# Kernel tuning notes

Measured on AMD Instinct MI355X. Metric: run time of the kernel, lower is better.

Reference implementation:

```python
import jax, jax.numpy as jnp
import numpy as np
import math

SEQ_LEN = 720
PRED_LEN = 720
CHANNELS = 862
BATCH = 64
IN_LEN = SEQ_LEN // 2  # seq_len is even -> no padding branch


def dct2_ortho_matrix(N):
    # Orthonormal DCT-II matrix D so that dct(x, norm='ortho') = x @ D.T along last axis
    n = jnp.arange(N, dtype=jnp.float32)
    k = n[:, None]
    D = jnp.cos(jnp.pi * (n[None, :] + 0.5) * k / N) * jnp.sqrt(2.0 / N)
    D = D.at[0].multiply(1.0 / jnp.sqrt(2.0))
    return D  # [N, N], row k = frequency k


def setup_inputs() -> dict:
    key = jax.random.key(0)
    ks = jax.random.split(key, 7)
    x = jax.random.normal(ks[0], (BATCH, SEQ_LEN, CHANNELS), dtype=jnp.float32)
    # depthwise 1x1 convs == per-channel scale + bias
    w1 = jax.random.normal(ks[1], (CHANNELS,), dtype=jnp.float32) * 0.1
    b1 = jax.random.normal(ks[2], (CHANNELS,), dtype=jnp.float32) * 0.1
    w2 = jax.random.normal(ks[3], (CHANNELS,), dtype=jnp.float32) * 0.1
    b2 = jax.random.normal(ks[4], (CHANNELS,), dtype=jnp.float32) * 0.1
    # Linear(in_len, pred_len): W [pred_len, in_len], b [pred_len]
    W_lo = jax.random.normal(ks[5], (PRED_LEN, IN_LEN), dtype=jnp.float32) / math.sqrt(IN_LEN)
    b_lo = jax.random.normal(ks[6], (PRED_LEN,), dtype=jnp.float32) * 0.01
    return {"x": x, "w1": w1, "b1": b1, "w2": w2, "b2": b2, "W_lo": W_lo, "b_lo": b_lo}


def reference(x, w1, b1, w2, b2, W_lo, b_lo):
    B, L, C = x.shape
    xt = jnp.transpose(x, (0, 2, 1))              # [B, C, L]
    seq_mean = jnp.mean(xt, axis=-1, keepdims=True)
    xt = xt - seq_mean
    # depthwise low-pass conv, kernel [1,1]/sqrt(2), stride 2
    lp = xt.reshape(B, C, L // 2, 2).sum(-1) / jnp.sqrt(jnp.float32(2.0))  # [B, C, N]
    N = L // 2
    D = dct2_ortho_matrix(N)
    xd = jnp.einsum('bcn,kn->bck', lp, D) / N     # DCT-II ortho along last axis, scaled
    # x += conv1x1_1(conv1x1_2(x)) -- depthwise 1x1 convs are per-channel affine
    y = (xd * w2[:, None] + b2[:, None]) * w1[:, None] + b1[:, None]
    xd = xd + y
    out = jnp.einsum('bcn,pn->bcp', xd, W_lo) + b_lo  # Linear(in_len -> pred_len)
    out = out + seq_mean                           # [B, C, pred_len]
    return jnp.transpose(out, (0, 2, 1))           # [B, pred_len, C]
```

## Files before the change

kernel.cpp:

```cpp
#include <hip/hip_runtime.h>
#include <hip/hip_bf16.h>
#include <cstdint>

#define SEQ   720
#define PRED  720
#define CH    862
#define NB    64
#define NIN   360
#define KP    384
#define CP    896
#define PP    768
#define BK    32

typedef __attribute__((ext_vector_type(8))) short s16x8;
typedef __attribute__((ext_vector_type(4))) float f32x4;
typedef __attribute__((ext_vector_type(2))) float f32x2;
typedef unsigned int u32;
typedef unsigned short u16;

__device__ __forceinline__ u16 to_bf16u(float f){
  __hip_bfloat16 h = __float2bfloat16(f);
  return *reinterpret_cast<u16*>(&h);
}

__global__ __launch_bounds__(256) void k_dct(float* __restrict__ Dm){
  int idx = blockIdx.x*256 + threadIdx.x;
  if (idx >= NIN*NIN) return;
  int n = idx / NIN, m = idx % NIN;
  int r = ((2*m+1)*n) % (4*NIN);
  float ang = (float)r * (float)(3.14159265358979323846 / 720.0);
  float v = cosf(ang) * 0.07453559924999299f;
  if (n == 0) v *= 0.7071067811865476f;
  Dm[idx] = v;
}

__global__ __launch_bounds__(384) void k_mmat(const float* __restrict__ Wlo, const float* __restrict__ Dm,
                                              u16* __restrict__ Mbf, float* __restrict__ Srow,
                                              float* __restrict__ Slo){
  int p = blockIdx.x;
  int t = threadIdx.x;
  if (p >= PRED){
    Mbf[(size_t)p*KP + t] = 0;
    if (t == 0){ Srow[p] = 0.f; Slo[p] = 0.f; }
    return;
  }
  __shared__ float Wrow[NIN];
  __shared__ float redM[6], redW[6];
  if (t < NIN) Wrow[t] = Wlo[(size_t)p*NIN + t];
  __syncthreads();
  float acc = 0.f;
  if (t < NIN){
    const float* Dc = Dm + t;
    #pragma unroll 4
    for (int n = 0; n < NIN; n++) acc += Wrow[n] * Dc[(size_t)n*NIN];
    acc *= (1.0f/360.0f);
  }
  Mbf[(size_t)p*KP + t] = (t < NIN) ? to_bf16u(acc) : (u16)0;
  float mv = (t < NIN) ? acc : 0.f;
  float wv = (t < NIN) ? Wrow[t] : 0.f;
  #pragma unroll
  for (int off = 32; off > 0; off >>= 1){
    mv += __shfl_down(mv, off);
    wv += __shfl_down(wv, off);
  }
  int wid = t >> 6, lid = t & 63;
  if (lid == 0){ redM[wid] = mv; redW[wid] = wv; }
  __syncthreads();
  if (t == 0){
    float sm = 0.f, sw = 0.f;
    #pragma unroll
    for (int i = 0; i < 6; i++){ sm += redM[i]; sw += redW[i]; }
    Srow[p] = sm; Slo[p] = sw;
  }
}

__global__ __launch_bounds__(256) void k_pre(const float* __restrict__ x, u16* __restrict__ pairB,
                                             float* __restrict__ meanw){
  int b  = blockIdx.y;
  int c0 = blockIdx.x * 64;
  int t  = threadIdx.x;
  int c16  = t & 15;
  int mrow = t >> 4;
  int w    = t >> 6;
  __shared__ u16  pl[NIN][66];
  __shared__ float red[4][64];
  const float rs2 = 0.7071067811865476f;
  int cb = c0 + c16*4;
  bool full = (cb + 3 < CH);
  const float* xb = x + (size_t)b*SEQ*CH + cb;
  float s0=0.f, s1=0.f, s2=0.f, s3=0.f;

  for (int m = mrow; m < NIN; m += 16){
    const float* r0 = xb + (size_t)(2*m)*CH;
    float a0,a1,a2,a3, e0,e1,e2,e3;
    if (full){
      f32x4 va = *reinterpret_cast<const f32x4*>(r0);
      f32x2 vb = *reinterpret_cast<const f32x2*>(r0 + CH);
      f32x2 vc = *reinterpret_cast<const f32x2*>(r0 + CH + 2);
      a0=va.x; a1=va.y; a2=va.z; a3=va.w;
      e0=vb.x; e1=vb.y; e2=vc.x; e3=vc.y;
    } else {
      a0 = (cb+0<CH)? r0[0]:0.f; a1 = (cb+1<CH)? r0[1]:0.f;
      a2 = (cb+2<CH)? r0[2]:0.f; a3 = (cb+3<CH)? r0[3]:0.f;
      e0 = (cb+0<CH)? r0[CH+0]:0.f; e1 = (cb+1<CH)? r0[CH+1]:0.f;
      e2 = (cb+2<CH)? r0[CH+2]:0.f; e3 = (cb+3<CH)? r0[CH+3]:0.f;
    }
    float p0=a0+e0, p1=a1+e1, p2=a2+e2, p3=a3+e3;
    s0+=p0; s1+=p1; s2+=p2; s3+=p3;
    u32 lo = (u32)to_bf16u(p0*rs2) | ((u32)to_bf16u(p1*rs2) << 16);
    u32 hi = (u32)to_bf16u(p2*rs2) | ((u32)to_bf16u(p3*rs2) << 16);
    *reinterpret_cast<u32*>(&pl[m][c16*4 + 0]) = lo;
    *reinterpret_cast<u32*>(&pl[m][c16*4 + 2]) = hi;
  }

  s0 += __shfl_down(s0, 32); s1 += __shfl_down(s1, 32);
  s2 += __shfl_down(s2, 32); s3 += __shfl_down(s3, 32);
  s0 += __shfl_down(s0, 16); s1 += __shfl_down(s1, 16);
  s2 += __shfl_down(s2, 16); s3 += __shfl_down(s3, 16);
  if ((t & 63) < 16){
    f32x4 rv; rv.x=s0; rv.y=s1; rv.z=s2; rv.w=s3;
    *reinterpret_cast<f32x4*>(&red[w][c16*4]) = rv;
  }
  __syncthreads();
  if (t < 64){
    float mean = (red[0][t] + red[1][t] + red[2][t] + red[3][t]) * (1.0f/SEQ);
    meanw[(size_t)b*CP + c0 + t] = mean;
  }

  int rowc = t >> 2;
  int mq0  = t & 3;
  size_t rbase = ((size_t)b*CP + c0 + rowc) * KP;
  for (int i = 0; i < 12; i++){
    int mg = mq0 + 4*i;
    u16 vals[8];
    #pragma unroll
    for (int j = 0; j < 8; j++){
      int m = mg*8 + j;
      vals[j] = (m < NIN) ? pl[m][rowc] : (u16)0;
    }
    uint4 pk;
    pk.x = (u32)vals[0] | ((u32)vals[1] << 16);
    pk.y = (u32)vals[2] | ((u32)vals[3] << 16);
    pk.z = (u32)vals[4] | ((u32)vals[5] << 16);
    pk.w = (u32)vals[6] | ((u32)vals[7] << 16);
    *reinterpret_cast<uint4*>(pairB + rbase + (size_t)mg*8) = pk;
  }
}

#define GLOAD_LDS16(gp, lp_) __builtin_amdgcn_global_load_lds( \
    (const __attribute__((address_space(1))) u32*)(gp), \
    (__attribute__((address_space(3))) u32*)(lp_), 16, 0, 0)

__global__ __launch_bounds__(256, 4) void k_gemm(const u16* __restrict__ Apack, const u16* __restrict__ Mbf,
                                              const float* __restrict__ Srow, const float* __restrict__ Slo,
                                              const float* __restrict__ meanw,
                                              const float* __restrict__ w1, const float* __restrict__ b1,
                                              const float* __restrict__ w2, const float* __restrict__ b2,
                                              const float* __restrict__ blo,
                                              float* __restrict__ out){
  int bid = blockIdx.x;
  int idx = (bid & 7) * 336 + (bid >> 3);
  int pt  = idx % 6;
  int rem = idx / 6;
  int ct  = rem % 7;
  int b   = rem / 7;

  int t  = threadIdx.x;
  int w  = t >> 6, l = t & 63;
  int wr = w >> 1, wc = w & 1;

  __shared__ __align__(16) char smem[32768];
  u16 (*As)[128*BK] = reinterpret_cast<u16(*)[128*BK]>(smem);
  u16 (*Bs)[128*BK] = reinterpret_cast<u16(*)[128*BK]>(smem + 16384);
  float (*wbuf)[16][68] = reinterpret_cast<float(*)[16][68]>(smem);

  f32x4 acc[4][4] = {};

  const u16* Abase = Apack + ((size_t)b*CP + (size_t)ct*128) * KP;
  const u16* Bbase = Mbf + (size_t)pt*128*KP;
  int srow = t >> 2;
  int squad = t & 3;
  int row16 = l & 15, kb = l >> 4;
  int sperm = (srow >> 1) & 3;
  int rperm = (row16 >> 1) & 3;

#define STAGE(bufi, k0) do { \
    GLOAD_LDS16(Abase + (size_t)(srow)*KP + (k0) + ((squad^sperm))*8,      &As[bufi][(srow)*BK + squad*8]); \
    GLOAD_LDS16(Abase + (size_t)(64 + srow)*KP + (k0) + ((squad^sperm))*8, &As[bufi][(64 + srow)*BK + squad*8]); \
    GLOAD_LDS16(Bbase + (size_t)(srow)*KP + (k0) + ((squad^sperm))*8,      &Bs[bufi][(srow)*BK + squad*8]); \
    GLOAD_LDS16(Bbase + (size_t)(64 + srow)*KP + (k0) + ((squad^sperm))*8, &Bs[bufi][(64 + srow)*BK + squad*8]); \
  } while(0)

  STAGE(0, 0);
  for (int ks = 0; ks < 12; ks++){
    int cur = ks & 1;
    if (ks < 11){
      STAGE(cur ^ 1, (ks + 1) * BK);
      asm volatile("s_waitcnt vmcnt(4)" ::: "memory");
    } else {
      asm volatile("s_waitcnt vmcnt(0)" ::: "memory");
    }
    __builtin_amdgcn_s_barrier();
    s16x8 af[4], bfr[4];
    #pragma unroll
    for (int mi = 0; mi < 4; mi++)
      af[mi] = *reinterpret_cast<const s16x8*>(&As[cur][(wr*64 + mi*16 + row16)*BK + (kb^rperm)*8]);
    #pragma unroll
    for (int ni = 0; ni < 4; ni++)
      bfr[ni] = *reinterpret_cast<const s16x8*>(&Bs[cur][(wc*64 + ni*16 + row16)*BK + (kb^rperm)*8]);
    __builtin_amdgcn_s_setprio(1);
    #pragma unroll
    for (int mi = 0; mi < 4; mi++)
      #pragma unroll
      for (int ni = 0; ni < 4; ni++)
        acc[mi][ni] = __builtin_amdgcn_mfma_f32_16x16x32_bf16(af[mi], bfr[ni], acc[mi][ni], 0, 0, 0);
    __builtin_amdgcn_s_setprio(0);
    __builtin_amdgcn_s_barrier();
  }
  __syncthreads();

  int cq = l & 15, pg = l >> 4;
  int cb4 = ct*128 + wr*64 + cq*4;
  float sc4[4], of4[4], cn4[4];
  float bc4[4];
  #pragma unroll
  for (int j = 0; j < 4; j++){
    int c = cb4 + j;
    bool v = (c < CH);
    float w1v = v ? w1[c] : 0.f, w2v = v ? w2[c] : 0.f;
    float b1v = v ? b1[c] : 0.f, b2v = v ? b2[c] : 0.f;
    float mv  = v ? meanw[(size_t)b*CP + c] : 0.f;
    sc4[j] = 1.f + w1v*w2v;
    of4[j] = w1v*b2v + b1v;
    cn4[j] = mv;
    bc4[j] = 1.4142135623730951f * sc4[j] * mv;
  }
  bool cfull = (cb4 + 3 < CH);
  size_t outb = (size_t)b*PRED*CH;

  #pragma unroll
  for (int ni = 0; ni < 4; ni++){
    #pragma unroll
    for (int mi = 0; mi < 4; mi++){
      #pragma unroll
      for (int r = 0; r < 4; r++){
        wbuf[w][row16][mi*16 + kb*4 + r] = acc[mi][ni][r];
      }
    }
    int pbase = pt*128 + wc*64 + ni*16;
    #pragma unroll
    for (int q = 0; q < 4; q++){
      int pi = q*4 + pg;
      int p = pbase + pi;
      if (p < PRED){
        f32x4 g = *reinterpret_cast<const f32x4*>(&wbuf[w][pi][cq*4]);
        float sp = Srow[p], sl = Slo[p], bl = blo[p];
        f32x4 ov;
        #pragma unroll
        for (int j = 0; j < 4; j++)
          ov[j] = sc4[j]*g[j] + (cn4[j] - bc4[j]*sp + of4[j]*sl + bl);
        if (cfull){
          *reinterpret_cast<f32x4*>(&out[outb + (size_t)p*CH + cb4]) = ov;
        } else {
          #pragma unroll
          for (int j = 0; j < 4; j++)
            if (cb4 + j < CH) out[outb + (size_t)p*CH + cb4 + j] = ov[j];
        }
      }
    }
  }
}

extern "C" void kernel_launch(void* const* d_in, const int* in_sizes, int n_in,
                              void* d_out, int out_size, void* d_ws, size_t ws_size,
                              hipStream_t stream)
{
  const float* x   = (const float*)d_in[0];
  const float* w1  = (const float*)d_in[1];
  const float* b1  = (const float*)d_in[2];
  const float* w2  = (const float*)d_in[3];
  const float* b2  = (const float*)d_in[4];
  const float* Wlo = (const float*)d_in[5];
  const float* blo = (const float*)d_in[6];
  float* out = (float*)d_out;

  char* ws = (char*)d_ws;
  float* Dm    = (float*)(ws);
  u16*   Mbf   = (u16*)(ws + 518400);
  float* Srow  = (float*)(ws + 518400 + 589824);
  float* Slo   = (float*)(ws + 518400 + 589824 + 3072);
  u16*   pairB = (u16*)(ws + 518400 + 589824 + 6144);
  float* meanw = (float*)(ws + 518400 + 589824 + 6144 + 44040192);

  k_dct<<<dim3((NIN*NIN + 255)/256), dim3(256), 0, stream>>>(Dm);
  k_mmat<<<dim3(PP), dim3(384), 0, stream>>>(Wlo, Dm, Mbf, Srow, Slo);
  k_pre<<<dim3(CP/64, NB), dim3(256), 0, stream>>>(x, pairB, meanw);
  k_gemm<<<dim3(6*7*NB), dim3(256), 0, stream>>>(pairB, Mbf, Srow, Slo, meanw,
                                                 w1, b1, w2, b2, blo, out);
}
```

Measured before the change: 162.8 us.

## Fuse preprocessing into GEMM, keeping full-K activation tile resident in LDS

Merges the pairwise-sum/mean/bf16-pack kernel with the GEMM. Each 512-thread block now loads a 64-channel slice of one batch from x, keeps the whole 384-long K panel in XOR-swizzled LDS, and loops over three 256-wide output tiles, streaming only the DCT-Linear matrix. This removes the packed intermediate buffer round-trip through global memory and one launch. The cost is 80KB of LDS per block, which limits occupancy, plus a serial prologue whose global loads of x are scalar and cannot overlap with the MFMA work.

```diff
diff --git a/kernel.cpp b/kernel.cpp
--- a/kernel.cpp
+++ b/kernel.cpp
@@ -8,13 +8,11 @@
 #define NB    64
 #define NIN   360
 #define KP    384
-#define CP    896
 #define PP    768
-#define BK    32
+#define BKK   32
 
 typedef __attribute__((ext_vector_type(8))) short s16x8;
 typedef __attribute__((ext_vector_type(4))) float f32x4;
-typedef __attribute__((ext_vector_type(2))) float f32x2;
 typedef unsigned int u32;
 typedef unsigned short u16;
 
@@ -74,200 +72,184 @@
   }
 }
 
-__global__ __launch_bounds__(256) void k_pre(const float* __restrict__ x, u16* __restrict__ pairB,
-                                             float* __restrict__ meanw){
-  int b  = blockIdx.y;
-  int c0 = blockIdx.x * 64;
-  int t  = threadIdx.x;
-  int c16  = t & 15;
-  int mrow = t >> 4;
-  int w    = t >> 6;
-  __shared__ u16  pl[NIN][66];
-  __shared__ float red[4][64];
-  const float rs2 = 0.7071067811865476f;
-  int cb = c0 + c16*4;
-  bool full = (cb + 3 < CH);
-  const float* xb = x + (size_t)b*SEQ*CH + cb;
-  float s0=0.f, s1=0.f, s2=0.f, s3=0.f;
-
-  for (int m = mrow; m < NIN; m += 16){
-    const float* r0 = xb + (size_t)(2*m)*CH;
-    float a0,a1,a2,a3, e0,e1,e2,e3;
-    if (full){
-      f32x4 va = *reinterpret_cast<const f32x4*>(r0);
-      f32x2 vb = *reinterpret_cast<const f32x2*>(r0 + CH);
-      f32x2 vc = *reinterpret_cast<const f32x2*>(r0 + CH + 2);
-      a0=va.x; a1=va.y; a2=va.z; a3=va.w;
-      e0=vb.x; e1=vb.y; e2=vc.x; e3=vc.y;
-    } else {
-      a0 = (cb+0<CH)? r0[0]:0.f; a1 = (cb+1<CH)? r0[1]:0.f;
-      a2 = (cb+2<CH)? r0[2]:0.f; a3 = (cb+3<CH)? r0[3]:0.f;
-      e0 = (cb+0<CH)? r0[CH+0]:0.f; e1 = (cb+1<CH)? r0[CH+1]:0.f;
-      e2 = (cb+2<CH)? r0[CH+2]:0.f; e3 = (cb+3<CH)? r0[CH+3]:0.f;
-    }
-    float p0=a0+e0, p1=a1+e1, p2=a2+e2, p3=a3+e3;
-    s0+=p0; s1+=p1; s2+=p2; s3+=p3;
-    u32 lo = (u32)to_bf16u(p0*rs2) | ((u32)to_bf16u(p1*rs2) << 16);
-    u32 hi = (u32)to_bf16u(p2*rs2) | ((u32)to_bf16u(p3*rs2) << 16);
-    *reinterpret_cast<u32*>(&pl[m][c16*4 + 0]) = lo;
-    *reinterpret_cast<u32*>(&pl[m][c16*4 + 2]) = hi;
-  }
-
-  s0 += __shfl_down(s0, 32); s1 += __shfl_down(s1, 32);
-  s2 += __shfl_down(s2, 32); s3 += __shfl_down(s3, 32);
-  s0 += __shfl_down(s0, 16); s1 += __shfl_down(s1, 16);
-  s2 += __shfl_down(s2, 16); s3 += __shfl_down(s3, 16);
-  if ((t & 63) < 16){
-    f32x4 rv; rv.x=s0; rv.y=s1; rv.z=s2; rv.w=s3;
-    *reinterpret_cast<f32x4*>(&red[w][c16*4]) = rv;
-  }
-  __syncthreads();
-  if (t < 64){
-    float mean = (red[0][t] + red[1][t] + red[2][t] + red[3][t]) * (1.0f/SEQ);
-    meanw[(size_t)b*CP + c0 + t] = mean;
-  }
-
-  int rowc = t >> 2;
-  int mq0  = t & 3;
-  size_t rbase = ((size_t)b*CP + c0 + rowc) * KP;
-  for (int i = 0; i < 12; i++){
-    int mg = mq0 + 4*i;
-    u16 vals[8];
-    #pragma unroll
-    for (int j = 0; j < 8; j++){
-      int m = mg*8 + j;
-      vals[j] = (m < NIN) ? pl[m][rowc] : (u16)0;
-    }
-    uint4 pk;
-    pk.x = (u32)vals[0] | ((u32)vals[1] << 16);
-    pk.y = (u32)vals[2] | ((u32)vals[3] << 16);
-    pk.z = (u32)vals[4] | ((u32)vals[5] << 16);
-    pk.w = (u32)vals[6] | ((u32)vals[7] << 16);
-    *reinterpret_cast<uint4*>(pairB + rbase + (size_t)mg*8) = pk;
-  }
-}
-
 #define GLOAD_LDS16(gp, lp_) __builtin_amdgcn_global_load_lds( \
     (const __attribute__((address_space(1))) u32*)(gp), \
     (__attribute__((address_space(3))) u32*)(lp_), 16, 0, 0)
 
-__global__ __launch_bounds__(256, 4) void k_gemm(const u16* __restrict__ Apack, const u16* __restrict__ Mbf,
-                                              const float* __restrict__ Srow, const float* __restrict__ Slo,
-                                              const float* __restrict__ meanw,
-                                              const float* __restrict__ w1, const float* __restrict__ b1,
-                                              const float* __restrict__ w2, const float* __restrict__ b2,
-                                              const float* __restrict__ blo,
-                                              float* __restrict__ out){
+__global__ __launch_bounds__(512, 4) void k_fused(
+    const float* __restrict__ x, const u16* __restrict__ Mbf,
+    const float* __restrict__ Srow, const float* __restrict__ Slo,
+    const float* __restrict__ w1, const float* __restrict__ b1,
+    const float* __restrict__ w2, const float* __restrict__ b2,
+    const float* __restrict__ blo, float* __restrict__ out)
+{
   int bid = blockIdx.x;
-  int idx = (bid & 7) * 336 + (bid >> 3);
-  int pt  = idx % 6;
-  int rem = idx / 6;
-  int ct  = rem % 7;
-  int b   = rem / 7;
-
-  int t  = threadIdx.x;
-  int w  = t >> 6, l = t & 63;
-  int wr = w >> 1, wc = w & 1;
-
-  __shared__ __align__(16) char smem[32768];
-  u16 (*As)[128*BK] = reinterpret_cast<u16(*)[128*BK]>(smem);
-  u16 (*Bs)[128*BK] = reinterpret_cast<u16(*)[128*BK]>(smem + 16384);
-  float (*wbuf)[16][68] = reinterpret_cast<float(*)[16][68]>(smem);
-
-  f32x4 acc[4][4] = {};
-
-  const u16* Abase = Apack + ((size_t)b*CP + (size_t)ct*128) * KP;
-  const u16* Bbase = Mbf + (size_t)pt*128*KP;
-  int srow = t >> 2;
-  int squad = t & 3;
-  int row16 = l & 15, kb = l >> 4;
-  int sperm = (srow >> 1) & 3;
-  int rperm = (row16 >> 1) & 3;
-
-#define STAGE(bufi, k0) do { \
-    GLOAD_LDS16(Abase + (size_t)(srow)*KP + (k0) + ((squad^sperm))*8,      &As[bufi][(srow)*BK + squad*8]); \
-    GLOAD_LDS16(Abase + (size_t)(64 + srow)*KP + (k0) + ((squad^sperm))*8, &As[bufi][(64 + srow)*BK + squad*8]); \
-    GLOAD_LDS16(Bbase + (size_t)(srow)*KP + (k0) + ((squad^sperm))*8,      &Bs[bufi][(srow)*BK + squad*8]); \
-    GLOAD_LDS16(Bbase + (size_t)(64 + srow)*KP + (k0) + ((squad^sperm))*8, &Bs[bufi][(64 + srow)*BK + squad*8]); \
-  } while(0)
-
-  STAGE(0, 0);
-  for (int ks = 0; ks < 12; ks++){
-    int cur = ks & 1;
-    if (ks < 11){
-      STAGE(cur ^ 1, (ks + 1) * BK);
-      asm volatile("s_waitcnt vmcnt(4)" ::: "memory");
-    } else {
-      asm volatile("s_waitcnt vmcnt(0)" ::: "memory");
-    }
-    __builtin_amdgcn_s_barrier();
-    s16x8 af[4], bfr[4];
-    #pragma unroll
-    for (int mi = 0; mi < 4; mi++)
-      af[mi] = *reinterpret_cast<const s16x8*>(&As[cur][(wr*64 + mi*16 + row16)*BK + (kb^rperm)*8]);
-    #pragma unroll
-    for (int ni = 0; ni < 4; ni++)
-      bfr[ni] = *reinterpret_cast<const s16x8*>(&Bs[cur][(wc*64 + ni*16 + row16)*BK + (kb^rperm)*8]);
-    __builtin_amdgcn_s_setprio(1);
-    #pragma unroll
-    for (int mi = 0; mi < 4; mi++)
-      #pragma unroll
-      for (int ni = 0; ni < 4; ni++)
-        acc[mi][ni] = __builtin_amdgcn_mfma_f32_16x16x32_bf16(af[mi], bfr[ni], acc[mi][ni], 0, 0, 0);
-    __builtin_amdgcn_s_setprio(0);
-    __builtin_amdgcn_s_barrier();
+  int ct = bid % 14;
+  int b  = bid / 14;
+  int c0 = ct * 64;
+
+  int t = threadIdx.x;
+  int w = t >> 6, l = t & 63;
+
+  __shared__ __align__(16) char smem[81920];
+  u16* As = (u16*)smem;
+  char* uni = smem + 49152;
+  u16* Bs0 = (u16*)uni;
+  u16* Bs1 = (u16*)(uni + 16384);
+  float (*red)[64]    = (float(*)[64])uni;
+  float* meansL       = (float*)(uni + 2048);
+  float (*wbuf)[8][68] = (float(*)[8][68])uni;
+
+  const float rs2 = 0.7071067811865476f;
+
+  int cglob = c0 + l;
+  bool cval = (cglob < CH);
+  const float* xb = x + (size_t)b*SEQ*CH + cglob;
+  float msum = 0.f;
+  int mbase = 48 * w;
+  #pragma unroll 1
+  for (int i8 = 0; i8 < 6; i8++){
+    u16 mb[8];
+    #pragma unroll
+    for (int j = 0; j < 8; j++){
+      int m = mbase + i8*8 + j;
+      float pr = 0.f;
+      if (m < NIN && cval){
+        size_t ro = (size_t)(2*m)*CH;
+        pr = xb[ro] + xb[ro + CH];
+      }
+      msum += pr;
+      mb[j] = to_bf16u(pr * rs2);
+    }
+    int ch   = (mbase >> 3) + i8;
+    int phys = ch ^ (l & 7);
+    uint4 pk;
+    pk.x = (u32)mb[0] | ((u32)mb[1] << 16);
+    pk.y = (u32)mb[2] | ((u32)mb[3] << 16);
+    pk.z = (u32)mb[4] | ((u32)mb[5] << 16);
+    pk.w = (u32)mb[6] | ((u32)mb[7] << 16);
+    *reinterpret_cast<uint4*>(As + (size_t)l*KP + phys*8) = pk;
+  }
+  red[w][l] = msum;
+  __syncthreads();
+  if (t < 64){
+    float s = 0.f;
+    #pragma unroll
+    for (int ww = 0; ww < 8; ww++) s += red[ww][t];
+    meansL[t] = s * (1.0f/SEQ);
   }
   __syncthreads();
 
   int cq = l & 15, pg = l >> 4;
-  int cb4 = ct*128 + wr*64 + cq*4;
-  float sc4[4], of4[4], cn4[4];
-  float bc4[4];
+  int cb4 = c0 + cq*4;
+  float sc4[4], of4[4], cn4[4], bc4[4];
   #pragma unroll
   for (int j = 0; j < 4; j++){
     int c = cb4 + j;
     bool v = (c < CH);
     float w1v = v ? w1[c] : 0.f, w2v = v ? w2[c] : 0.f;
     float b1v = v ? b1[c] : 0.f, b2v = v ? b2[c] : 0.f;
-    float mv  = v ? meanw[(size_t)b*CP + c] : 0.f;
+    float mv = meansL[cq*4 + j];
     sc4[j] = 1.f + w1v*w2v;
     of4[j] = w1v*b2v + b1v;
     cn4[j] = mv;
     bc4[j] = 1.4142135623730951f * sc4[j] * mv;
   }
   bool cfull = (cb4 + 3 < CH);
+  __syncthreads();
+
+  int srow2 = t >> 2;
+  int sq    = t & 3;
+  int bperm = (srow2 >> 1) & 3;
+  int r16 = l & 15, kb = l >> 4;
+  int rpermB = (r16 >> 1) & 3;
   size_t outb = (size_t)b*PRED*CH;
 
-  #pragma unroll
-  for (int ni = 0; ni < 4; ni++){
-    #pragma unroll
-    for (int mi = 0; mi < 4; mi++){
-      #pragma unroll
-      for (int r = 0; r < 4; r++){
-        wbuf[w][row16][mi*16 + kb*4 + r] = acc[mi][ni][r];
+#define STAGE_B(dst, p0_, k0_) do { \
+    GLOAD_LDS16(Mbf + (size_t)((p0_) + srow2)*KP + (k0_) + ((sq^bperm)*8),        (dst) + srow2*BKK + sq*8); \
+    GLOAD_LDS16(Mbf + (size_t)((p0_) + 128 + srow2)*KP + (k0_) + ((sq^bperm)*8),  (dst) + (128+srow2)*BKK + sq*8); \
+  } while(0)
+
+  #pragma unroll 1
+  for (int pt = 0; pt < 3; pt++){
+    int p0 = pt * 256;
+    float spv[8], slv[8], blv[8];
+    #pragma unroll
+    for (int hq = 0; hq < 8; hq++){
+      int p = p0 + w*32 + (hq>>2)*16 + ((hq>>1)&1)*8 + (hq&1)*4 + pg;
+      p = (p < PRED) ? p : (PRED-1);
+      spv[hq] = Srow[p]; slv[hq] = Slo[p]; blv[hq] = blo[p];
+    }
+
+    f32x4 acc[4][2] = {};
+    STAGE_B(Bs0, p0, 0);
+    #pragma unroll 1
+    for (int ks = 0; ks < 12; ks++){
+      u16* Bc = (ks & 1) ? Bs1 : Bs0;
+      u16* Bn = (ks & 1) ? Bs0 : Bs1;
+      if (ks < 11){
+        STAGE_B(Bn, p0, (ks+1)*BKK);
+        asm volatile("s_waitcnt vmcnt(2)" ::: "memory");
+      } else {
+        asm volatile("s_waitcnt vmcnt(0)" ::: "memory");
       }
-    }
-    int pbase = pt*128 + wc*64 + ni*16;
-    #pragma unroll
-    for (int q = 0; q < 4; q++){
-      int pi = q*4 + pg;
-      int p = pbase + pi;
-      if (p < PRED){
-        f32x4 g = *reinterpret_cast<const f32x4*>(&wbuf[w][pi][cq*4]);
-        float sp = Srow[p], sl = Slo[p], bl = blo[p];
-        f32x4 ov;
+      __builtin_amdgcn_s_barrier();
+      s16x8 af[4], bfr[2];
+      int ch0 = ks*4;
+      #pragma unroll
+      for (int mi = 0; mi < 4; mi++)
+        af[mi] = *reinterpret_cast<const s16x8*>(As + (size_t)(mi*16 + r16)*KP + (((ch0 + kb) ^ (l & 7)))*8);
+      #pragma unroll
+      for (int ni = 0; ni < 2; ni++)
+        bfr[ni] = *reinterpret_cast<const s16x8*>(Bc + (size_t)(w*32 + ni*16 + r16)*BKK + ((kb ^ rpermB))*8);
+      __builtin_amdgcn_s_setprio(1);
+      #pragma unroll
+      for (int mi = 0; mi < 4; mi++)
         #pragma unroll
-        for (int j = 0; j < 4; j++)
-          ov[j] = sc4[j]*g[j] + (cn4[j] - bc4[j]*sp + of4[j]*sl + bl);
-        if (cfull){
-          *reinterpret_cast<f32x4*>(&out[outb + (size_t)p*CH + cb4]) = ov;
-        } else {
+        for (int ni = 0; ni < 2; ni++)
+          acc[mi][ni] = __builtin_amdgcn_mfma_f32_16x16x32_bf16(af[mi], bfr[ni], acc[mi][ni], 0, 0, 0);
+      __builtin_amdgcn_s_setprio(0);
+      __builtin_amdgcn_s_barrier();
+    }
+    __syncthreads();
+
+    #pragma unroll
+    for (int ni = 0; ni < 2; ni++){
+      #pragma unroll
+      for (int half = 0; half < 2; half++){
+        asm volatile("s_waitcnt lgkmcnt(0)" ::: "memory");
+        if ((r16 >> 3) == half){
           #pragma unroll
-          for (int j = 0; j < 4; j++)
-            if (cb4 + j < CH) out[outb + (size_t)p*CH + cb4 + j] = ov[j];
+          for (int mi = 0; mi < 4; mi++)
+            #pragma unroll
+            for (int r = 0; r < 4; r++)
+              wbuf[w][r16 & 7][mi*16 + kb*4 + r] = acc[mi][ni][r];
+        }
+        asm volatile("s_waitcnt lgkmcnt(0)" ::: "memory");
+        #pragma unroll
+        for (int q = 0; q < 2; q++){
+          int pi = q*4 + pg;
+          int p = p0 + w*32 + ni*16 + half*8 + pi;
+          if (p < PRED && cb4 < CH){
+            f32x4 g = *reinterpret_cast<const f32x4*>(&wbuf[w][pi][cq*4]);
+            int hq = ni*4 + half*2 + q;
+            float sp = spv[hq], sl = slv[hq], bl = blv[hq];
+            f32x4 ov;
+            #pragma unroll
+            for (int j = 0; j < 4; j++)
+              ov[j] = sc4[j]*g[j] + (cn4[j] - bc4[j]*sp + of4[j]*sl + bl);
+            if (cfull){
+              *reinterpret_cast<f32x4*>(&out[outb + (size_t)p*CH + cb4]) = ov;
+            } else {
+              #pragma unroll
+              for (int j = 0; j < 4; j++)
+                if (cb4 + j < CH) out[outb + (size_t)p*CH + cb4 + j] = ov[j];
+            }
+          }
         }
       }
     }
+    __syncthreads();
   }
 }
 
@@ -289,12 +271,9 @@
   u16*   Mbf   = (u16*)(ws + 518400);
   float* Srow  = (float*)(ws + 518400 + 589824);
   float* Slo   = (float*)(ws + 518400 + 589824 + 3072);
-  u16*   pairB = (u16*)(ws + 518400 + 589824 + 6144);
-  float* meanw = (float*)(ws + 518400 + 589824 + 6144 + 44040192);
 
   k_dct<<<dim3((NIN*NIN + 255)/256), dim3(256), 0, stream>>>(Dm);
   k_mmat<<<dim3(PP), dim3(384), 0, stream>>>(Wlo, Dm, Mbf, Srow, Slo);
-  k_pre<<<dim3(CP/64, NB), dim3(256), 0, stream>>>(x, pairB, meanw);
-  k_gemm<<<dim3(6*7*NB), dim3(256), 0, stream>>>(pairB, Mbf, Srow, Slo, meanw,
+  k_fused<<<dim3(NB*14), dim3(512), 0, stream>>>(x, Mbf, Srow, Slo,
                                                  w1, b1, w2, b2, blo, out);
 }
```

After: 188.8 us. 1.16x slower.
